# Optimization experiments

Measured on AMD Instinct MI355X. Metric: run time of the kernel, lower is better.

The kernel has to match this reference:

```python
import jax, jax.numpy as jnp
import numpy as np

D = 1024
HEADS = 16
HEAD_DIM = D // HEADS
EPS = 1e-5


def layer_norm(x, gamma, beta):
    mu = jnp.mean(x, axis=-1, keepdims=True)
    var = jnp.mean(jnp.square(x - mu), axis=-1, keepdims=True)
    return (x - mu) * jax.lax.rsqrt(var + EPS) * gamma + beta


def setup_inputs() -> dict:
    key = jax.random.key(0)
    ks = jax.random.split(key, 8)
    B, S = 4, 2048
    s_in = 1.0 / np.sqrt(D)
    s_ffn = 1.0 / np.sqrt(4 * D)
    return {
        "x": jax.random.normal(ks[0], (B, S, D), dtype=jnp.float32),
        "ln1_g": jnp.ones((D,), jnp.float32),
        "ln1_b": jnp.zeros((D,), jnp.float32),
        "w_qkv": jax.random.uniform(ks[1], (D, 3 * D), jnp.float32, -s_in, s_in),
        "b_qkv": jnp.zeros((3 * D,), jnp.float32),
        "w_out": jax.random.uniform(ks[2], (D, D), jnp.float32, -s_in, s_in),
        "b_out": jnp.zeros((D,), jnp.float32),
        "ln2_g": jnp.ones((D,), jnp.float32),
        "ln2_b": jnp.zeros((D,), jnp.float32),
        "w_ffn1": jax.random.uniform(ks[3], (D, 4 * D), jnp.float32, -s_in, s_in),
        "b_ffn1": jnp.zeros((4 * D,), jnp.float32),
        "w_ffn2": jax.random.uniform(ks[4], (4 * D, D), jnp.float32, -s_ffn, s_ffn),
        "b_ffn2": jnp.zeros((D,), jnp.float32),
    }


def reference(x, ln1_g, ln1_b, w_qkv, b_qkv, w_out, b_out,
              ln2_g, ln2_b, w_ffn1, b_ffn1, w_ffn2, b_ffn2):
    B, S, Dm = x.shape
    h = layer_norm(x, ln1_g, ln1_b)
    qkv = h @ w_qkv + b_qkv  # [B,S,3D]
    q, k, v = jnp.split(qkv, 3, axis=-1)
    # [B,S,D] -> [B,H,S,hd]
    def to_heads(t):
        return t.reshape(B, S, HEADS, HEAD_DIM).transpose(0, 2, 1, 3)
    q, k, v = to_heads(q), to_heads(k), to_heads(v)
    scores = jnp.einsum('bhqd,bhkd->bhqk', q, k) / np.sqrt(HEAD_DIM).astype(np.float32)
    attn = jax.nn.softmax(scores, axis=-1)
    out = jnp.einsum('bhqk,bhkd->bhqd', attn, v)
    out = out.transpose(0, 2, 1, 3).reshape(B, S, Dm)
    x = x + (out @ w_out + b_out)
    h = layer_norm(x, ln2_g, ln2_b)
    h = jax.nn.gelu(h @ w_ffn1 + b_ffn1, approximate=False) @ w_ffn2 + b_ffn2
    return x + h
```

## Files before the change

kernel.cpp:

```cpp
#include <hip/hip_runtime.h>
#include <cstdint>
#include <cstddef>

typedef unsigned short u16;
typedef unsigned int   u32;
typedef __bf16 bf16x8 __attribute__((ext_vector_type(8)));
typedef float  f32x4  __attribute__((ext_vector_type(4)));
static_assert(sizeof(bf16x8) == 16, "bf16x8 must be 16B");
static_assert(sizeof(f32x4) == 16, "f32x4 must be 16B");

#define DEVI static __device__ __forceinline__

#define QSCALE 0.18033688011112042f

DEVI u16 f2bf(float x) {
  u32 u = __builtin_bit_cast(u32, x);
  u = (u + 0x7FFFu + ((u >> 16) & 1u)) >> 16;
  return (u16)u;
}

DEVI void gload16(const u16* g, u16* l) {
  __builtin_amdgcn_global_load_lds(
      (const __attribute__((address_space(1))) void*)g,
      (__attribute__((address_space(3))) void*)l, 16, 0, 0);
}

#define S_BARRIER() asm volatile("s_barrier" ::: "memory")
#define VMCNT(n) asm volatile("s_waitcnt vmcnt(" #n ")" ::: "memory")

template <int MO, int NACC>
DEVI void mm16(f32x4 (&acc)[NACC][4], const bf16x8 (&af)[4], const bf16x8 (&bf)[4]) {
  __builtin_amdgcn_s_setprio(1);
#pragma unroll
  for (int m = 0; m < 4; m++)
#pragma unroll
    for (int n = 0; n < 4; n++)
      acc[MO + m][n] =
          __builtin_amdgcn_mfma_f32_16x16x32_bf16(af[m], bf[n], acc[MO + m][n], 0, 0, 0);
  __builtin_amdgcn_s_setprio(0);
}

__global__ __launch_bounds__(256) void transpose_cvt(const float* __restrict__ W,
                                                     u16* __restrict__ WT,
                                                     int K, int N,
                                                     float scale, int nscale) {
  __shared__ float tile[32][33];
  int tx = threadIdx.x & 31, ty = threadIdx.x >> 5;
  int c0 = blockIdx.x * 32, r0 = blockIdx.y * 32;
#pragma unroll
  for (int i = 0; i < 4; i++)
    tile[ty + i * 8][tx] = W[(size_t)(r0 + ty + i * 8) * N + c0 + tx];
  __syncthreads();
#pragma unroll
  for (int i = 0; i < 4; i++) {
    int r = ty + i * 8;
    int n = c0 + r;
    float scl = (n < nscale) ? scale : 1.f;
    WT[(size_t)n * K + r0 + tx] = f2bf(tile[tx][r] * scl);
  }
}

__global__ __launch_bounds__(256) void prep_bias(const float* __restrict__ b,
                                                 float* __restrict__ o) {
  int i = blockIdx.x * 256 + threadIdx.x;
  o[i] = b[i] * (i < 1024 ? QSCALE : 1.f);
}

__global__ __launch_bounds__(256) void ln_k(const float* __restrict__ X,
                                            const float* __restrict__ gam,
                                            const float* __restrict__ bet,
                                            u16* __restrict__ H) {
  __shared__ float2 part[4];
  int row = blockIdx.x, t = threadIdx.x;
  const float4* xr = (const float4*)(X + (size_t)row * 1024);
  float4 v = xr[t];
  float s = v.x + v.y + v.z + v.w;
  float q = v.x * v.x + v.y * v.y + v.z * v.z + v.w * v.w;
#pragma unroll
  for (int o = 32; o > 0; o >>= 1) {
    s += __shfl_xor(s, o);
    q += __shfl_xor(q, o);
  }
  if ((t & 63) == 0) part[t >> 6] = make_float2(s, q);
  __syncthreads();
  float S = part[0].x + part[1].x + part[2].x + part[3].x;
  float Q = part[0].y + part[1].y + part[2].y + part[3].y;
  float mu = S * (1.f / 1024.f);
  float rs = rsqrtf(Q * (1.f / 1024.f) - mu * mu + 1e-5f);
  float4 gv = ((const float4*)gam)[t];
  float4 bv = ((const float4*)bet)[t];
  ushort4 o;
  o.x = f2bf((v.x - mu) * rs * gv.x + bv.x);
  o.y = f2bf((v.y - mu) * rs * gv.y + bv.y);
  o.z = f2bf((v.z - mu) * rs * gv.z + bv.z);
  o.w = f2bf((v.w - mu) * rs * gv.w + bv.w);
  *(ushort4*)(H + (size_t)row * 1024 + t * 4) = o;
}

template <int EPI, int NACC>
DEVI void epilogue(f32x4 (&acc)[NACC][4], const float* bias, const float* res,
                   float* outF, u16* outB, int N, int rbase, int cbase, int g, int li) {
#pragma unroll
  for (int n = 0; n < 4; n++) {
    int c = cbase + n * 16 + li;
    float bv = bias[c];
#pragma unroll
    for (int a = 0; a < NACC; a++) {
      int rowb = rbase + a * 16 + g * 4;
#pragma unroll
      for (int r = 0; r < 4; r++) {
        size_t idx = (size_t)(rowb + r) * N + c;
        float v = acc[a][n][r] + bv;
        if constexpr (EPI == 1) {
          v += res[idx];
          outF[idx] = v;
        } else if constexpr (EPI == 2) {
          v = 0.5f * v * (1.f + erff(v * 0.70710678118654752f));
          outB[idx] = f2bf(v);
        } else {
          outB[idx] = f2bf(v);
        }
      }
    }
  }
}

template <int EPI>
__global__ __launch_bounds__(512, 1) void gemm256(const u16* __restrict__ A,
                                                  const u16* __restrict__ Bt,
                                                  const float* __restrict__ bias,
                                                  const float* __restrict__ res,
                                                  float* __restrict__ outF,
                                                  u16* __restrict__ outB,
                                                  int M, int N, int K) {
  __shared__ uint4 As[2][2048];
  __shared__ uint4 Bs[2][2048];
  const int t = threadIdx.x, lane = t & 63, wv = t >> 6;
  const int wr = wv >> 2, wc = wv & 3;
  const int li = lane & 15, g = lane >> 4;

  const int gx = gridDim.x;
  const int nwg = gx * gridDim.y;
  const int wg = blockIdx.y * gx + blockIdx.x;
  const int swz = (wg & 7) * (nwg >> 3) + (wg >> 3);
  const int bx = swz % gx, by = swz / gx;
  const int bm0 = by * 256, bn0 = bx * 256;

  f32x4 acc[8][4];
  const f32x4 z4 = {0.f, 0.f, 0.f, 0.f};
#pragma unroll
  for (int a = 0; a < 8; a++)
#pragma unroll
    for (int n = 0; n < 4; n++) acc[a][n] = z4;

  const u16* aB = A + (size_t)(bm0 + wv * 16 + li) * K + g * 8;
  const u16* bB = Bt + (size_t)(bn0 + wv * 16 + li) * K + g * 8;
  const size_t rskip = (size_t)128 * K;

  auto stA = [&](int buf, int j, int kt) {
    gload16(aB + (size_t)kt * 64 + ((j & 1) ? rskip : (size_t)0) + (j >> 1) * 32,
            (u16*)&As[buf][(j * 8 + wv) * 64]);
  };
  auto stB = [&](int buf, int j, int kt) {
    gload16(bB + (size_t)kt * 64 + ((j & 1) ? rskip : (size_t)0) + (j >> 1) * 32,
            (u16*)&Bs[buf][(j * 8 + wv) * 64]);
  };

  stA(0, 0, 0); stA(0, 1, 0); stB(0, 0, 0); stB(0, 1, 0);
  stA(0, 2, 0); stA(0, 3, 0); stB(0, 2, 0); stB(0, 3, 0);
  VMCNT(4);
  S_BARRIER();

  const int NT = K >> 6;
  int cur = 0;
  for (int kt = 0; kt < NT; kt++) {
    const int nx = cur ^ 1;
    const bool more = (kt + 1 < NT);
    bf16x8 af[4], bf[4];
#pragma unroll
    for (int n = 0; n < 4; n++)
      bf[n] = __builtin_bit_cast(bf16x8, Bs[cur][(wc * 4 + n) * 64 + lane]);
#pragma unroll
    for (int m = 0; m < 4; m++)
      af[m] = __builtin_bit_cast(bf16x8, As[cur][(wr * 8 + m) * 64 + lane]);
    if (more) { stA(nx, 0, kt + 1); stA(nx, 1, kt + 1); }
    S_BARRIER();
    mm16<0>(acc, af, bf);
    S_BARRIER();
#pragma unroll
    for (int m = 0; m < 4; m++)
      af[m] = __builtin_bit_cast(bf16x8, As[cur][(wr * 8 + 4 + m) * 64 + lane]);
    if (more) { stB(nx, 0, kt + 1); stB(nx, 1, kt + 1); }
    S_BARRIER();
    mm16<4>(acc, af, bf);
    if (more) { VMCNT(4); } else { VMCNT(0); }
    S_BARRIER();
#pragma unroll
    for (int n = 0; n < 4; n++)
      bf[n] = __builtin_bit_cast(bf16x8, Bs[cur][(16 + wc * 4 + n) * 64 + lane]);
#pragma unroll
    for (int m = 0; m < 4; m++)
      af[m] = __builtin_bit_cast(bf16x8, As[cur][(16 + wr * 8 + m) * 64 + lane]);
    if (more) { stA(nx, 2, kt + 1); stA(nx, 3, kt + 1); }
    S_BARRIER();
    mm16<0>(acc, af, bf);
    S_BARRIER();
#pragma unroll
    for (int m = 0; m < 4; m++)
      af[m] = __builtin_bit_cast(bf16x8, As[cur][(16 + wr * 8 + 4 + m) * 64 + lane]);
    if (more) { stB(nx, 2, kt + 1); stB(nx, 3, kt + 1); }
    S_BARRIER();
    mm16<4>(acc, af, bf);
    if (more) { VMCNT(4); }
    S_BARRIER();
    cur = nx;
  }

  epilogue<EPI>(acc, bias, res, outF, outB, N, bm0 + wr * 128, bn0 + wc * 64, g, li);
}

template <int EPI>
__global__ __launch_bounds__(512, 1) void gemm128(const u16* __restrict__ A,
                                                  const u16* __restrict__ Bt,
                                                  const float* __restrict__ bias,
                                                  const float* __restrict__ res,
                                                  float* __restrict__ outF,
                                                  u16* __restrict__ outB,
                                                  int M, int N, int K) {
  __shared__ uint4 As[2][1024];
  __shared__ uint4 Bs[2][2048];
  const int t = threadIdx.x, lane = t & 63, wv = t >> 6;
  const int wr = wv >> 2, wc = wv & 3;
  const int li = lane & 15, g = lane >> 4;

  const int gx = gridDim.x;
  const int nwg = gx * gridDim.y;
  const int wg = blockIdx.y * gx + blockIdx.x;
  const int swz = (wg & 7) * (nwg >> 3) + (wg >> 3);
  const int bx = swz % gx, by = swz / gx;
  const int bm0 = by * 128, bn0 = bx * 256;

  f32x4 acc[4][4];
  const f32x4 z4 = {0.f, 0.f, 0.f, 0.f};
#pragma unroll
  for (int a = 0; a < 4; a++)
#pragma unroll
    for (int n = 0; n < 4; n++) acc[a][n] = z4;

  const u16* aB = A + (size_t)(bm0 + wv * 16 + li) * K + g * 8;
  const u16* bB = Bt + (size_t)(bn0 + wv * 16 + li) * K + g * 8;
  const size_t rskip = (size_t)128 * K;

  auto stA = [&](int buf, int j, int kt) {
    gload16(aB + (size_t)kt * 64 + j * 32, (u16*)&As[buf][(j * 8 + wv) * 64]);
  };
  auto stB = [&](int buf, int j, int kt) {
    gload16(bB + (size_t)kt * 64 + ((j & 1) ? rskip : (size_t)0) + (j >> 1) * 32,
            (u16*)&Bs[buf][(j * 8 + wv) * 64]);
  };

  stA(0, 0, 0); stB(0, 0, 0); stB(0, 1, 0);
  stA(0, 1, 0); stB(0, 2, 0); stB(0, 3, 0);
  VMCNT(3);
  S_BARRIER();

  const int NT = K >> 6;
  int cur = 0;
  for (int kt = 0; kt < NT; kt++) {
    const int nx = cur ^ 1;
    const bool more = (kt + 1 < NT);
    bf16x8 af[4], bf[4];
#pragma unroll
    for (int n = 0; n < 4; n++)
      bf[n] = __builtin_bit_cast(bf16x8, Bs[cur][(wc * 4 + n) * 64 + lane]);
#pragma unroll
    for (int m = 0; m < 4; m++)
      af[m] = __builtin_bit_cast(bf16x8, As[cur][(wr * 4 + m) * 64 + lane]);
    if (more) { stA(nx, 0, kt + 1); stB(nx, 0, kt + 1); stB(nx, 1, kt + 1); }
    S_BARRIER();
    mm16<0>(acc, af, bf);
    if (more) { VMCNT(3); } else { VMCNT(0); }
    S_BARRIER();
#pragma unroll
    for (int n = 0; n < 4; n++)
      bf[n] = __builtin_bit_cast(bf16x8, Bs[cur][(16 + wc * 4 + n) * 64 + lane]);
#pragma unroll
    for (int m = 0; m < 4; m++)
      af[m] = __builtin_bit_cast(bf16x8, As[cur][(8 + wr * 4 + m) * 64 + lane]);
    if (more) { stA(nx, 1, kt + 1); stB(nx, 2, kt + 1); stB(nx, 3, kt + 1); }
    S_BARRIER();
    mm16<0>(acc, af, bf);
    if (more) { VMCNT(3); }
    S_BARRIER();
    cur = nx;
  }

  epilogue<EPI>(acc, bias, res, outF, outB, N, bm0 + wr * 64, bn0 + wc * 64, g, li);
}

__global__ __launch_bounds__(256) void v_tr(const u16* __restrict__ qkv,
                                            u16* __restrict__ vfm) {
  __shared__ u16 Vl[64 * 72];
  const int t = threadIdx.x;
  const int bh = blockIdx.y;
  const int bb = bh >> 4, h = bh & 15;
  const int kt = blockIdx.x;
#pragma unroll
  for (int bq = 0; bq < 2; bq++) {
    int c = t + bq * 256;
    int key = c >> 3, d0 = (c & 7) * 8;
    uint4 v = *(const uint4*)(qkv + (size_t)(bb * 2048 + kt * 64 + key) * 3072 + 2048 +
                              h * 64 + d0);
    *(uint4*)&Vl[key * 72 + d0] = v;
  }
  __syncthreads();
#pragma unroll
  for (int bq = 0; bq < 2; bq++) {
    int oc = t + bq * 256;
    int f = oc >> 6, l = oc & 63;
    int db = f >> 1, g32 = f & 1;
    int li = l & 15, g = l >> 4;
    u16 tmp[8];
#pragma unroll
    for (int e = 0; e < 8; e++) {
      int pk = g32 * 32 + ((e & 4) << 2) + g * 4 + (e & 3);
      tmp[e] = Vl[pk * 72 + db * 16 + li];
    }
    *(uint4*)(vfm + ((((size_t)bh * 32 + kt) * 8 + f) * 64 + l) * 8) = *(uint4*)tmp;
  }
}

__global__ __launch_bounds__(256) void attn_k(const u16* __restrict__ qkv,
                                              const u16* __restrict__ vfm,
                                              u16* __restrict__ ao) {
  __shared__ uint4 Ks[1024];
  __shared__ uint4 Vs[1024];
  const int t = threadIdx.x, lane = t & 63, wv = t >> 6;
  const int g = lane >> 4, li = lane & 15;
  const int bb = blockIdx.y >> 4, h = blockIdx.y & 15;
  const int q0 = blockIdx.x * 64 + wv * 16;

  const size_t qoff = (size_t)(bb * 2048 + q0 + li) * 3072 + h * 64 + g * 8;
  bf16x8 qf0 = __builtin_bit_cast(bf16x8, *(const uint4*)(qkv + qoff));
  bf16x8 qf1 = __builtin_bit_cast(bf16x8, *(const uint4*)(qkv + qoff + 32));

  const u16* kbase = qkv + (size_t)bb * 2048 * 3072 + 1024 + h * 64;
  const u16* ksrc[4];
  const u16* vsrc[4];
  const u16* vbase = vfm + (size_t)(bb * 16 + h) * 32 * 4096;
#pragma unroll
  for (int j = 0; j < 4; j++) {
    int f = wv + j * 4;
    ksrc[j] = kbase + (size_t)(((f >> 1) << 4) + li) * 3072 + ((f & 1) << 5) + g * 8;
    vsrc[j] = vbase + (size_t)(f >> 3) * 4096 + ((f & 7) * 64 + lane) * 8;
  }

  const f32x4 z4 = {0.f, 0.f, 0.f, 0.f};
  f32x4 Of[4];
#pragma unroll
  for (int db = 0; db < 4; db++) Of[db] = z4;
  float m_run = -INFINITY, l_run = 0.f;

  for (int tile = 0; tile < 16; tile++) {
    __syncthreads();
#pragma unroll
    for (int j = 0; j < 4; j++) {
      int f = wv + j * 4;
      gload16(ksrc[j] + (size_t)tile * 128 * 3072, (u16*)&Ks[f * 64]);
      gload16(vsrc[j] + (size_t)tile * 8192, (u16*)&Vs[f * 64]);
    }
    __syncthreads();

    float sc[32];
    float mt = -INFINITY;
#pragma unroll
    for (int kb = 0; kb < 8; kb++) {
      bf16x8 k0f = __builtin_bit_cast(bf16x8, Ks[(kb * 2 + 0) * 64 + lane]);
      bf16x8 k1f = __builtin_bit_cast(bf16x8, Ks[(kb * 2 + 1) * 64 + lane]);
      f32x4 st = z4;
      st = __builtin_amdgcn_mfma_f32_16x16x32_bf16(k0f, qf0, st, 0, 0, 0);
      st = __builtin_amdgcn_mfma_f32_16x16x32_bf16(k1f, qf1, st, 0, 0, 0);
      const int g32 = kb >> 1, tt = kb & 1;
#pragma unroll
      for (int r = 0; r < 4; r++) {
        float s = st[r];
        sc[g32 * 8 + tt * 4 + r] = s;
        mt = fmaxf(mt, s);
      }
    }
    mt = fmaxf(mt, __shfl_xor(mt, 16));
    mt = fmaxf(mt, __shfl_xor(mt, 32));

    if (!__all(mt - m_run <= 8.f)) {
      float mn = fmaxf(m_run, mt);
      float aa = exp2f(m_run - mn);
      l_run *= aa;
      float a0 = __shfl(aa, g * 4 + 0);
      float a1 = __shfl(aa, g * 4 + 1);
      float a2 = __shfl(aa, g * 4 + 2);
      float a3 = __shfl(aa, g * 4 + 3);
#pragma unroll
      for (int db = 0; db < 4; db++) {
        Of[db][0] *= a0;
        Of[db][1] *= a1;
        Of[db][2] *= a2;
        Of[db][3] *= a3;
      }
      m_run = mn;
    }

    float ps = 0.f;
#pragma unroll
    for (int i = 0; i < 32; i++) {
      float p = exp2f(sc[i] - m_run);
      sc[i] = p;
      ps += p;
    }
    ps += __shfl_xor(ps, 16);
    ps += __shfl_xor(ps, 32);
    l_run += ps;

#pragma unroll
    for (int g32 = 0; g32 < 4; g32++) {
      bf16x8 pf;
#pragma unroll
      for (int j = 0; j < 8; j++) pf[j] = (__bf16)sc[g32 * 8 + j];
      const int fb = (g32 >> 1) * 8 + (g32 & 1);
#pragma unroll
      for (int db = 0; db < 4; db++) {
        bf16x8 vf = __builtin_bit_cast(bf16x8, Vs[(fb + db * 2) * 64 + lane]);
        Of[db] = __builtin_amdgcn_mfma_f32_16x16x32_bf16(pf, vf, Of[db], 0, 0, 0);
      }
    }
  }

  float invl[4];
#pragma unroll
  for (int r = 0; r < 4; r++) invl[r] = 1.f / __shfl(l_run, g * 4 + r);
#pragma unroll
  for (int db = 0; db < 4; db++)
#pragma unroll
    for (int r = 0; r < 4; r++)
      ao[(size_t)(bb * 2048 + q0 + 4 * g + r) * 1024 + h * 64 + db * 16 + li] =
          f2bf(Of[db][r] * invl[r]);
}

extern "C" void kernel_launch(void* const* d_in, const int* in_sizes, int n_in,
                              void* d_out, int out_size, void* d_ws, size_t ws_size,
                              hipStream_t stream) {
  const float* x = (const float*)d_in[0];
  const float* ln1g = (const float*)d_in[1];
  const float* ln1b = (const float*)d_in[2];
  const float* wqkv = (const float*)d_in[3];
  const float* bqkv = (const float*)d_in[4];
  const float* wout = (const float*)d_in[5];
  const float* bout = (const float*)d_in[6];
  const float* ln2g = (const float*)d_in[7];
  const float* ln2b = (const float*)d_in[8];
  const float* wff1 = (const float*)d_in[9];
  const float* bff1 = (const float*)d_in[10];
  const float* wff2 = (const float*)d_in[11];
  const float* bff2 = (const float*)d_in[12];
  float* outF = (float*)d_out;
  char* ws = (char*)d_ws;

  u16* wqkvT = (u16*)(ws + 0);
  u16* woutT = (u16*)(ws + 6291456);
  u16* wff1T = (u16*)(ws + 8388608);
  u16* wff2T = (u16*)(ws + 16777216);
  u16* hbuf  = (u16*)(ws + 25165824);
  u16* vfm   = (u16*)(ws + 25165824);
  u16* qkvb  = (u16*)(ws + 41943040);
  u16* attnb = (u16*)(ws + 92274688);
  u16* ffn1b = qkvb;
  float* biasq = (float*)attnb;

  transpose_cvt<<<dim3(96, 32), 256, 0, stream>>>(wqkv, wqkvT, 1024, 3072, QSCALE, 1024);
  transpose_cvt<<<dim3(32, 32), 256, 0, stream>>>(wout, woutT, 1024, 1024, 1.f, 0);
  transpose_cvt<<<dim3(128, 32), 256, 0, stream>>>(wff1, wff1T, 1024, 4096, 1.f, 0);
  transpose_cvt<<<dim3(32, 128), 256, 0, stream>>>(wff2, wff2T, 4096, 1024, 1.f, 0);
  prep_bias<<<12, 256, 0, stream>>>(bqkv, biasq);

  ln_k<<<8192, 256, 0, stream>>>(x, ln1g, ln1b, hbuf);
  gemm256<0><<<dim3(12, 32), 512, 0, stream>>>(hbuf, wqkvT, biasq, nullptr, nullptr, qkvb,
                                               8192, 3072, 1024);
  v_tr<<<dim3(32, 64), 256, 0, stream>>>(qkvb, vfm);
  attn_k<<<dim3(32, 64), 256, 0, stream>>>(qkvb, vfm, attnb);
  gemm128<1><<<dim3(4, 64), 512, 0, stream>>>(attnb, woutT, bout, x, outF, nullptr,
                                              8192, 1024, 1024);
  ln_k<<<8192, 256, 0, stream>>>(outF, ln2g, ln2b, hbuf);
  gemm256<2><<<dim3(16, 32), 512, 0, stream>>>(hbuf, wff1T, bff1, nullptr, nullptr, ffn1b,
                                               8192, 4096, 1024);
  gemm128<1><<<dim3(4, 64), 512, 0, stream>>>(ffn1b, wff2T, bff2, outF, outF, nullptr,
                                              8192, 1024, 4096);

  (void)in_sizes;
  (void)n_in;
  (void)out_size;
  (void)ws_size;
}
```

Measured before the change: 497.1 us.

## Double-buffer K/V tiles in attention and compute row sums via MFMA

Result: slower. 526.1 us (+5.8%).

```diff
diff --git a/kernel.cpp b/kernel.cpp
--- a/kernel.cpp
+++ b/kernel.cpp
@@ -333,8 +333,8 @@
 __global__ __launch_bounds__(256) void attn_k(const u16* __restrict__ qkv,
                                               const u16* __restrict__ vfm,
                                               u16* __restrict__ ao) {
-  __shared__ uint4 Ks[1024];
-  __shared__ uint4 Vs[1024];
+  __shared__ uint4 Ks[2][1024];
+  __shared__ uint4 Vs[2][1024];
   const int t = threadIdx.x, lane = t & 63, wv = t >> 6;
   const int g = lane >> 4, li = lane & 15;
   const int bb = blockIdx.y >> 4, h = blockIdx.y & 15;
@@ -359,24 +359,36 @@
   f32x4 Of[4];
 #pragma unroll
   for (int db = 0; db < 4; db++) Of[db] = z4;
-  float m_run = -INFINITY, l_run = 0.f;
-
-  for (int tile = 0; tile < 16; tile++) {
-    __syncthreads();
+  f32x4 Ol = z4;
+  float m_run = -INFINITY;
+
+  bf16x8 vone;
+#pragma unroll
+  for (int j = 0; j < 8; j++) vone[j] = (__bf16)1.0f;
+
+  const int NT = 16;
+  auto stage = [&](int buf, int tile) {
 #pragma unroll
     for (int j = 0; j < 4; j++) {
       int f = wv + j * 4;
-      gload16(ksrc[j] + (size_t)tile * 128 * 3072, (u16*)&Ks[f * 64]);
-      gload16(vsrc[j] + (size_t)tile * 8192, (u16*)&Vs[f * 64]);
-    }
-    __syncthreads();
-
+      gload16(ksrc[j] + (size_t)tile * 128 * 3072, (u16*)&Ks[buf][f * 64]);
+      gload16(vsrc[j] + (size_t)tile * 8192, (u16*)&Vs[buf][f * 64]);
+    }
+  };
+  stage(0, 0);
+  stage(1, 1);
+  VMCNT(8);
+  S_BARRIER();
+
+  int cur = 0;
+  for (int tile = 0; tile < NT; tile++) {
     float sc[32];
     float mt = -INFINITY;
+    __builtin_amdgcn_s_setprio(1);
 #pragma unroll
     for (int kb = 0; kb < 8; kb++) {
-      bf16x8 k0f = __builtin_bit_cast(bf16x8, Ks[(kb * 2 + 0) * 64 + lane]);
-      bf16x8 k1f = __builtin_bit_cast(bf16x8, Ks[(kb * 2 + 1) * 64 + lane]);
+      bf16x8 k0f = __builtin_bit_cast(bf16x8, Ks[cur][(kb * 2 + 0) * 64 + lane]);
+      bf16x8 k1f = __builtin_bit_cast(bf16x8, Ks[cur][(kb * 2 + 1) * 64 + lane]);
       f32x4 st = z4;
       st = __builtin_amdgcn_mfma_f32_16x16x32_bf16(k0f, qf0, st, 0, 0, 0);
       st = __builtin_amdgcn_mfma_f32_16x16x32_bf16(k1f, qf1, st, 0, 0, 0);
@@ -388,13 +400,13 @@
         mt = fmaxf(mt, s);
       }
     }
+    __builtin_amdgcn_s_setprio(0);
     mt = fmaxf(mt, __shfl_xor(mt, 16));
     mt = fmaxf(mt, __shfl_xor(mt, 32));
 
     if (!__all(mt - m_run <= 8.f)) {
       float mn = fmaxf(m_run, mt);
       float aa = exp2f(m_run - mn);
-      l_run *= aa;
       float a0 = __shfl(aa, g * 4 + 0);
       float a1 = __shfl(aa, g * 4 + 1);
       float a2 = __shfl(aa, g * 4 + 2);
@@ -406,19 +418,12 @@
         Of[db][2] *= a2;
         Of[db][3] *= a3;
       }
+      Ol[0] *= a0; Ol[1] *= a1; Ol[2] *= a2; Ol[3] *= a3;
       m_run = mn;
     }
 
-    float ps = 0.f;
-#pragma unroll
-    for (int i = 0; i < 32; i++) {
-      float p = exp2f(sc[i] - m_run);
-      sc[i] = p;
-      ps += p;
-    }
-    ps += __shfl_xor(ps, 16);
-    ps += __shfl_xor(ps, 32);
-    l_run += ps;
+#pragma unroll
+    for (int i = 0; i < 32; i++) sc[i] = exp2f(sc[i] - m_run);
 
 #pragma unroll
     for (int g32 = 0; g32 < 4; g32++) {
@@ -426,17 +431,31 @@
 #pragma unroll
       for (int j = 0; j < 8; j++) pf[j] = (__bf16)sc[g32 * 8 + j];
       const int fb = (g32 >> 1) * 8 + (g32 & 1);
+      __builtin_amdgcn_s_setprio(1);
 #pragma unroll
       for (int db = 0; db < 4; db++) {
-        bf16x8 vf = __builtin_bit_cast(bf16x8, Vs[(fb + db * 2) * 64 + lane]);
+        bf16x8 vf = __builtin_bit_cast(bf16x8, Vs[cur][(fb + db * 2) * 64 + lane]);
         Of[db] = __builtin_amdgcn_mfma_f32_16x16x32_bf16(pf, vf, Of[db], 0, 0, 0);
       }
-    }
+      Ol = __builtin_amdgcn_mfma_f32_16x16x32_bf16(pf, vone, Ol, 0, 0, 0);
+      __builtin_amdgcn_s_setprio(0);
+    }
+
+    S_BARRIER();
+    if (tile + 2 < NT) {
+      stage(cur, tile + 2);
+      VMCNT(8);
+      S_BARRIER();
+    } else if (tile + 1 < NT) {
+      VMCNT(0);
+      S_BARRIER();
+    }
+    cur ^= 1;
   }
 
   float invl[4];
 #pragma unroll
-  for (int r = 0; r < 4; r++) invl[r] = 1.f / __shfl(l_run, g * 4 + r);
+  for (int r = 0; r < 4; r++) invl[r] = 1.f / Ol[r];
 #pragma unroll
   for (int db = 0; db < 4; db++)
 #pragma unroll
```
